# Optimization experiments

Hardware: AMD Instinct MI355X
Metric: run time of the kernel (lower is better)

## Reference

```python
import jax, jax.numpy as jnp
import numpy as np

B, S, D, H = 2, 2048, 1024, 16
HD = D // H  # 64


def setup_inputs() -> dict:
    key = jax.random.key(0)
    ks = jax.random.split(key, 10)
    sd = 1.0 / np.sqrt(D)
    return {
        "query": jax.random.normal(ks[0], (B, S, D), jnp.float32),
        "key": jax.random.normal(ks[1], (B, S, D), jnp.float32),
        "value": jax.random.normal(ks[2], (B, S, D), jnp.float32),
        "mask": jax.random.randint(ks[3], (B, S, S), 0, 2).astype(bool),
        "Wq": jax.random.normal(ks[4], (D, D), jnp.float32) * sd,
        "bq": jnp.zeros((D,), jnp.float32),
        "Wk": jax.random.normal(ks[5], (D, D), jnp.float32) * sd,
        "bk": jnp.zeros((D,), jnp.float32),
        "Wv": jax.random.normal(ks[6], (D, D), jnp.float32) * sd,
        "bv": jnp.zeros((D,), jnp.float32),
    }


def _split_heads(x, W, b):
    # nn.Linear: x @ W.T + b, then [B,S,D] -> [B*H,S,HD] (b-major, h-minor)
    h = x @ W.T + b
    h = h.reshape(B, S, H, HD).transpose(0, 2, 1, 3)  # [B,H,S,HD]
    return h.reshape(B * H, S, HD)


def reference(query, key, value, mask, Wq, bq, Wk, bk, Wv, bv):
    scale = np.sqrt(HD).astype(np.float32)
    q = _split_heads(query, Wq, bq)
    k = _split_heads(key, Wk, bk)
    v = _split_heads(value, Wv, bv)
    scores = jnp.einsum("bqd,bkd->bqk", q, k) / scale  # [B*H,S,S]
    # faithful to torch mask.repeat(H,1,1): tiles batch-major
    mask_r = jnp.tile(mask, (H, 1, 1))
    scores = jnp.where(mask_r, -jnp.inf, scores)
    attn = jax.nn.softmax(scores, axis=-1)
    ctx = jnp.einsum("bqk,bkd->bqd", attn, v)  # [B*H,S,HD]
    ctx = ctx.reshape(B, H, S, HD).transpose(0, 2, 1, 3).reshape(B, S, D)
    return ctx, attn
```

## Files before the change

### kernel.cpp

```cpp
#include <hip/hip_runtime.h>

#define B_ 2
#define S_ 2048
#define D_ 1024
#define H_ 16
#define HD_ 64
#define BH_ 32

typedef float fx4 __attribute__((ext_vector_type(4)));
typedef short s16x8 __attribute__((ext_vector_type(8)));
typedef unsigned short u16x8 __attribute__((ext_vector_type(8)));
typedef unsigned short u16x4 __attribute__((ext_vector_type(4)));

#define MFMA16(a, b, c) __builtin_amdgcn_mfma_f32_16x16x32_bf16((a), (b), (c), 0, 0, 0)

__device__ __forceinline__ unsigned short f2bf(float x) {
    unsigned u = __float_as_uint(x);
    return (unsigned short)((u + 0x7FFFu + ((u >> 16) & 1u)) >> 16);
}
__device__ __forceinline__ float bf2f(unsigned short h) {
    return __uint_as_float(((unsigned)h) << 16);
}

__global__ __launch_bounds__(256) void mask_pack(const int* __restrict__ m,
                                                 unsigned long long* __restrict__ out) {
    size_t i = (size_t)blockIdx.x * 256 + threadIdx.x;
    unsigned long long b = __ballot(m[i] != 0);
    if ((threadIdx.x & 63) == 0) out[i >> 6] = b;
}

template <int VMODE>
__global__ __launch_bounds__(256) void proj_mfma(
    const float* __restrict__ X, const float* __restrict__ W, const float* __restrict__ bias,
    unsigned short* __restrict__ o_hi, unsigned short* __restrict__ o_lo) {
    __shared__ __align__(16) unsigned short Ah[128 * 72];
    __shared__ __align__(16) unsigned short Al[128 * 72];
    __shared__ __align__(16) unsigned short Bh[64 * 72];
    __shared__ __align__(16) unsigned short Bl[64 * 72];

    const int t = threadIdx.x;
    const int n0 = blockIdx.x * 64;
    const int m0 = blockIdx.y * 128;
    const int wid = t >> 6, l = t & 63;
    const int wm = wid >> 1, wn = wid & 1;
    const int lr = l & 15, lq = l >> 4;

    fx4 acc[4][2];
#pragma unroll
    for (int i = 0; i < 4; ++i)
#pragma unroll
        for (int j = 0; j < 2; ++j) acc[i][j] = (fx4){0.f, 0.f, 0.f, 0.f};

    for (int k0 = 0; k0 < D_; k0 += 64) {
#pragma unroll
        for (int j = 0; j < 8; ++j) {
            int u = t + j * 256;
            int row = u >> 4, c4 = (u & 15) * 4;
            float4 f = *(const float4*)(X + (size_t)(m0 + row) * D_ + k0 + c4);
            unsigned short h0 = f2bf(f.x), h1 = f2bf(f.y), h2 = f2bf(f.z), h3 = f2bf(f.w);
            u16x4 hv = {h0, h1, h2, h3};
            u16x4 lv = {f2bf(f.x - bf2f(h0)), f2bf(f.y - bf2f(h1)),
                        f2bf(f.z - bf2f(h2)), f2bf(f.w - bf2f(h3))};
            *(u16x4*)(Ah + row * 72 + c4) = hv;
            *(u16x4*)(Al + row * 72 + c4) = lv;
        }
#pragma unroll
        for (int j = 0; j < 4; ++j) {
            int u = t + j * 256;
            int row = u >> 4, c4 = (u & 15) * 4;
            float4 f = *(const float4*)(W + (size_t)(n0 + row) * D_ + k0 + c4);
            unsigned short h0 = f2bf(f.x), h1 = f2bf(f.y), h2 = f2bf(f.z), h3 = f2bf(f.w);
            u16x4 hv = {h0, h1, h2, h3};
            u16x4 lv = {f2bf(f.x - bf2f(h0)), f2bf(f.y - bf2f(h1)),
                        f2bf(f.z - bf2f(h2)), f2bf(f.w - bf2f(h3))};
            *(u16x4*)(Bh + row * 72 + c4) = hv;
            *(u16x4*)(Bl + row * 72 + c4) = lv;
        }
        __syncthreads();
#pragma unroll
        for (int c = 0; c < 2; ++c) {
            s16x8 a_h[4], a_l[4];
#pragma unroll
            for (int mf = 0; mf < 4; ++mf) {
                int ro = (wm * 64 + mf * 16 + lr) * 72 + c * 32 + lq * 8;
                a_h[mf] = *(const s16x8*)(Ah + ro);
                a_l[mf] = *(const s16x8*)(Al + ro);
            }
#pragma unroll
            for (int nf = 0; nf < 2; ++nf) {
                int ro = (wn * 32 + nf * 16 + lr) * 72 + c * 32 + lq * 8;
                s16x8 b_h = *(const s16x8*)(Bh + ro);
                s16x8 b_l = *(const s16x8*)(Bl + ro);
#pragma unroll
                for (int mf = 0; mf < 4; ++mf) {
                    acc[mf][nf] = MFMA16(a_h[mf], b_h, acc[mf][nf]);
                    acc[mf][nf] = MFMA16(a_h[mf], b_l, acc[mf][nf]);
                    acc[mf][nf] = MFMA16(a_l[mf], b_h, acc[mf][nf]);
                }
            }
        }
        __syncthreads();
    }

    if (VMODE == 0) {
#pragma unroll
        for (int nf = 0; nf < 2; ++nf) {
            int n = n0 + wn * 32 + nf * 16 + lr;
            float bv = bias[n];
            int h = n >> 6, hd = n & 63;
#pragma unroll
            for (int mf = 0; mf < 4; ++mf)
#pragma unroll
                for (int r = 0; r < 4; ++r) {
                    int m = m0 + wm * 64 + mf * 16 + lq * 4 + r;
                    int b = m >> 11, s = m & 2047;
                    float v = acc[mf][nf][r] + bv;
                    size_t idx = ((size_t)((b * H_ + h) * S_ + s)) * HD_ + hd;
                    unsigned short hh = f2bf(v);
                    o_hi[idx] = hh;
                    o_lo[idx] = f2bf(v - bf2f(hh));
                }
        }
    } else {
        unsigned short* T = Ah;
#pragma unroll
        for (int nf = 0; nf < 2; ++nf) {
            int nl = wn * 32 + nf * 16 + lr;
            float bv = bias[n0 + nl];
#pragma unroll
            for (int mf = 0; mf < 4; ++mf)
#pragma unroll
                for (int r = 0; r < 4; ++r) {
                    int ml = wm * 64 + mf * 16 + lq * 4 + r;
                    T[nl * 136 + ml] = f2bf(acc[mf][nf][r] + bv);
                }
        }
        __syncthreads();
        int h = n0 >> 6, b = m0 >> 11, s0 = m0 & 2047;
        int hd = t >> 2, seg = t & 3;
        unsigned short* gp =
            o_hi + ((size_t)((b * H_ + h) * HD_ + hd)) * S_ + s0 + seg * 32;
#pragma unroll
        for (int j = 0; j < 4; ++j)
            *(u16x8*)(gp + j * 8) = *(const u16x8*)(T + hd * 136 + seg * 32 + j * 8);
    }
}

__global__ __launch_bounds__(256) void attn_mfma(
    const unsigned short* __restrict__ qh_g, const unsigned short* __restrict__ ql_g,
    const unsigned short* __restrict__ kh_g, const unsigned short* __restrict__ kl_g,
    const unsigned short* __restrict__ vt_g, const unsigned long long* __restrict__ pm,
    float* __restrict__ ctx, float* __restrict__ attn) {
    __shared__ __align__(16) unsigned short Kh[64 * 72];
    __shared__ __align__(16) unsigned short Kl[64 * 72];
    __shared__ __align__(16) unsigned short VT[64 * 72];
    __shared__ __align__(16) float E[64 * 68];

    const int t = threadIdx.x;
    const int wid = t >> 6, l = t & 63, lr = l & 15, lq = l >> 4;
    const int q0 = blockIdx.x * 64;
    const int bh = blockIdx.y;
    const size_t base = (size_t)bh * S_ * HD_;
    const size_t mrow_base = (size_t)(bh & (B_ - 1)) * S_;

    s16x8 qhi[2], qlo[2];
    {
        const unsigned short* p = qh_g + base + (size_t)(q0 + wid * 16 + lr) * HD_ + lq * 8;
        qhi[0] = *(const s16x8*)p;
        qhi[1] = *(const s16x8*)(p + 32);
        const unsigned short* p2 = ql_g + base + (size_t)(q0 + wid * 16 + lr) * HD_ + lq * 8;
        qlo[0] = *(const s16x8*)p2;
        qlo[1] = *(const s16x8*)(p2 + 32);
    }

    float rs[4] = {0.f, 0.f, 0.f, 0.f};

    for (int kt = 0; kt < S_; kt += 64) {
#pragma unroll
        for (int j = 0; j < 2; ++j) {
            int u = t + j * 256;
            int row = u >> 3, c8 = (u & 7) * 8;
            *(u16x8*)(Kh + row * 72 + c8) =
                *(const u16x8*)(kh_g + base + (size_t)(kt + row) * HD_ + c8);
        }
        __syncthreads();
        fx4 acc[4];
#pragma unroll
        for (int nt = 0; nt < 4; ++nt) acc[nt] = (fx4){0.f, 0.f, 0.f, 0.f};
#pragma unroll
        for (int c = 0; c < 2; ++c)
#pragma unroll
            for (int nt = 0; nt < 4; ++nt) {
                s16x8 kb = *(const s16x8*)(Kh + (nt * 16 + lr) * 72 + c * 32 + lq * 8);
                acc[nt] = MFMA16(qhi[c], kb, acc[nt]);
            }
        unsigned long long mw[4];
#pragma unroll
        for (int r = 0; r < 4; ++r)
            mw[r] = pm[(mrow_base + q0 + wid * 16 + lq * 4 + r) * (S_ / 64) + (kt >> 6)];
#pragma unroll
        for (int nt = 0; nt < 4; ++nt)
#pragma unroll
            for (int r = 0; r < 4; ++r) {
                float e = __expf(acc[nt][r] * 0.125f);
                e = ((mw[r] >> (nt * 16 + lr)) & 1ull) ? 0.f : e;
                rs[r] += e;
            }
        __syncthreads();
    }
#pragma unroll
    for (int off = 1; off < 16; off <<= 1)
#pragma unroll
        for (int r = 0; r < 4; ++r) rs[r] += __shfl_xor(rs[r], off, 16);
    float inv[4];
#pragma unroll
    for (int r = 0; r < 4; ++r) inv[r] = 1.f / rs[r];

    fx4 pacc[4];
#pragma unroll
    for (int dt = 0; dt < 4; ++dt) pacc[dt] = (fx4){0.f, 0.f, 0.f, 0.f};

    for (int kt = 0; kt < S_; kt += 64) {
#pragma unroll
        for (int j = 0; j < 2; ++j) {
            int u = t + j * 256;
            int row = u >> 3, c8 = (u & 7) * 8;
            *(u16x8*)(Kh + row * 72 + c8) =
                *(const u16x8*)(kh_g + base + (size_t)(kt + row) * HD_ + c8);
            *(u16x8*)(Kl + row * 72 + c8) =
                *(const u16x8*)(kl_g + base + (size_t)(kt + row) * HD_ + c8);
            *(u16x8*)(VT + row * 72 + c8) =
                *(const u16x8*)(vt_g + (size_t)(bh * HD_ + row) * S_ + kt + c8);
        }
        __syncthreads();
        fx4 acc[4];
#pragma unroll
        for (int nt = 0; nt < 4; ++nt) acc[nt] = (fx4){0.f, 0.f, 0.f, 0.f};
#pragma unroll
        for (int c = 0; c < 2; ++c)
#pragma unroll
            for (int nt = 0; nt < 4; ++nt) {
                int ro = (nt * 16 + lr) * 72 + c * 32 + lq * 8;
                s16x8 kbh = *(const s16x8*)(Kh + ro);
                s16x8 kbl = *(const s16x8*)(Kl + ro);
                acc[nt] = MFMA16(qhi[c], kbh, acc[nt]);
                acc[nt] = MFMA16(qhi[c], kbl, acc[nt]);
                acc[nt] = MFMA16(qlo[c], kbh, acc[nt]);
            }
        unsigned long long mw[4];
#pragma unroll
        for (int r = 0; r < 4; ++r)
            mw[r] = pm[(mrow_base + q0 + wid * 16 + lq * 4 + r) * (S_ / 64) + (kt >> 6)];
#pragma unroll
        for (int nt = 0; nt < 4; ++nt)
#pragma unroll
            for (int r = 0; r < 4; ++r) {
                float e = __expf(acc[nt][r] * 0.125f);
                e = ((mw[r] >> (nt * 16 + lr)) & 1ull) ? 0.f : e;
                E[(wid * 16 + lq * 4 + r) * 68 + nt * 16 + lr] = e * inv[r];
            }
        __syncthreads();
#pragma unroll
        for (int c = 0; c < 2; ++c) {
            const float* ep = E + (wid * 16 + lr) * 68 + c * 32 + lq * 8;
            fx4 p0 = *(const fx4*)ep;
            fx4 p1 = *(const fx4*)(ep + 4);
            s16x8 pa;
#pragma unroll
            for (int i = 0; i < 4; ++i) {
                pa[i] = (short)f2bf(p0[i]);
                pa[i + 4] = (short)f2bf(p1[i]);
            }
#pragma unroll
            for (int dt = 0; dt < 4; ++dt) {
                s16x8 vb = *(const s16x8*)(VT + (dt * 16 + lr) * 72 + c * 32 + lq * 8);
                pacc[dt] = MFMA16(pa, vb, pacc[dt]);
            }
        }
        {
            int rr = t >> 2, seg = t & 3;
            float* gout = attn + ((size_t)bh * S_ + q0 + rr) * S_ + kt + seg * 16;
            const float* ep2 = E + rr * 68 + seg * 16;
#pragma unroll
            for (int j = 0; j < 4; ++j) *(fx4*)(gout + j * 4) = *(const fx4*)(ep2 + j * 4);
        }
        __syncthreads();
    }

    const int b = bh >> 4, h = bh & 15;
#pragma unroll
    for (int dt = 0; dt < 4; ++dt)
#pragma unroll
        for (int r = 0; r < 4; ++r) {
            int q = q0 + wid * 16 + lq * 4 + r;
            ctx[((size_t)(b * S_ + q)) * D_ + h * HD_ + dt * 16 + lr] = pacc[dt][r];
        }
}

extern "C" void kernel_launch(void* const* d_in, const int* in_sizes, int n_in,
                              void* d_out, int out_size, void* d_ws, size_t ws_size,
                              hipStream_t stream) {
    (void)in_sizes; (void)n_in; (void)out_size; (void)ws_size;
    const float* q_in = (const float*)d_in[0];
    const float* k_in = (const float*)d_in[1];
    const float* v_in = (const float*)d_in[2];
    const int* mask = (const int*)d_in[3];
    const float* Wq = (const float*)d_in[4];
    const float* bq = (const float*)d_in[5];
    const float* Wk = (const float*)d_in[6];
    const float* bk = (const float*)d_in[7];
    const float* Wv = (const float*)d_in[8];
    const float* bv = (const float*)d_in[9];

    const size_t E_ = (size_t)BH_ * S_ * HD_;
    unsigned short* qh = (unsigned short*)d_ws;
    unsigned short* ql = qh + E_;
    unsigned short* kh = ql + E_;
    unsigned short* kl = kh + E_;
    unsigned short* vt = kl + E_;
    unsigned long long* pmask = (unsigned long long*)(vt + E_);

    float* ctx = (float*)d_out;
    float* attn = ctx + (size_t)B_ * S_ * D_;

    mask_pack<<<dim3((B_ * S_ * S_) / 256), dim3(256), 0, stream>>>(mask, pmask);

    dim3 pgrid(D_ / 64, (B_ * S_) / 128);
    proj_mfma<0><<<pgrid, dim3(256), 0, stream>>>(q_in, Wq, bq, qh, ql);
    proj_mfma<0><<<pgrid, dim3(256), 0, stream>>>(k_in, Wk, bk, kh, kl);
    proj_mfma<1><<<pgrid, dim3(256), 0, stream>>>(v_in, Wv, bv, vt, nullptr);

    dim3 agrid(S_ / 64, BH_);
    attn_mfma<<<agrid, dim3(256), 0, stream>>>(qh, ql, kh, kl, vt, pmask, ctx, attn);
}
```

Measured before the change: 1.104 ms.

## Pre-split inputs to bf16, use direct-to-LDS loads, and restructure attention tiling

Adds a conversion kernel that splits X and W into bf16 hi/lo pairs ahead of each projection. The projection GEMM then fills LDS with global_load_lds instead of converting per tile. The softmax scale times log2(e) is folded into Wq and bq so attention can call exp2 directly. V is stored in 64x64 tile-blocked layout, and attention now covers 128 queries per block (32 per wave), reading K and V straight from global memory and using only per-wave LDS for P, with wave barriers replacing block barriers. Attn values are written directly from registers. The cost is extra global traffic from the pre-converted buffers and uncoalesced per-lane attn stores.

```diff
diff --git a/kernel.cpp b/kernel.cpp
--- a/kernel.cpp
+++ b/kernel.cpp
@@ -12,7 +12,18 @@
 typedef unsigned short u16x8 __attribute__((ext_vector_type(8)));
 typedef unsigned short u16x4 __attribute__((ext_vector_type(4)));
 
+typedef __attribute__((address_space(1))) unsigned int uint_as1;
+typedef __attribute__((address_space(3))) unsigned int uint_as3;
+
 #define MFMA16(a, b, c) __builtin_amdgcn_mfma_f32_16x16x32_bf16((a), (b), (c), 0, 0, 0)
+
+#define QSCALE 0.18033688011112042f
+
+#if __has_builtin(__builtin_amdgcn_exp2f)
+#define EXP2F(x) __builtin_amdgcn_exp2f(x)
+#else
+#define EXP2F(x) exp2f(x)
+#endif
 
 __device__ __forceinline__ unsigned short f2bf(float x) {
     unsigned u = __float_as_uint(x);
@@ -20,6 +31,9 @@
 }
 __device__ __forceinline__ float bf2f(unsigned short h) {
     return __uint_as_float(((unsigned)h) << 16);
+}
+__device__ __forceinline__ void g2lds16(const unsigned short* g, unsigned short* l) {
+    __builtin_amdgcn_global_load_lds((uint_as1*)g, (uint_as3*)l, 16, 0, 0);
 }
 
 __global__ __launch_bounds__(256) void mask_pack(const int* __restrict__ m,
@@ -29,14 +43,40 @@
     if ((threadIdx.x & 63) == 0) out[i >> 6] = b;
 }
 
+__global__ __launch_bounds__(256) void cvt_pair(
+    const float* __restrict__ x, unsigned short* __restrict__ xh, unsigned short* __restrict__ xl,
+    const float* __restrict__ w, unsigned short* __restrict__ wh, unsigned short* __restrict__ wl,
+    float wscale) {
+    const int NX4 = (B_ * S_ * D_) / 4;
+    int i = blockIdx.x * 256 + threadIdx.x;
+    const float* src;
+    unsigned short* oh;
+    unsigned short* ol;
+    float sc;
+    int off;
+    if (i < NX4) { src = x; oh = xh; ol = xl; sc = 1.f; off = i; }
+    else         { src = w; oh = wh; ol = wl; sc = wscale; off = i - NX4; }
+    float4 f = ((const float4*)src)[off];
+    float a0 = f.x * sc, a1 = f.y * sc, a2 = f.z * sc, a3 = f.w * sc;
+    unsigned short h0 = f2bf(a0), h1 = f2bf(a1), h2 = f2bf(a2), h3 = f2bf(a3);
+    u16x4 hv = {h0, h1, h2, h3};
+    u16x4 lv = {f2bf(a0 - bf2f(h0)), f2bf(a1 - bf2f(h1)), f2bf(a2 - bf2f(h2)),
+                f2bf(a3 - bf2f(h3))};
+    *(u16x4*)(oh + (size_t)off * 4) = hv;
+    *(u16x4*)(ol + (size_t)off * 4) = lv;
+}
+
 template <int VMODE>
 __global__ __launch_bounds__(256) void proj_mfma(
-    const float* __restrict__ X, const float* __restrict__ W, const float* __restrict__ bias,
+    const unsigned short* __restrict__ Xh, const unsigned short* __restrict__ Xl,
+    const unsigned short* __restrict__ Wh, const unsigned short* __restrict__ Wl,
+    const float* __restrict__ bias, float bscale,
     unsigned short* __restrict__ o_hi, unsigned short* __restrict__ o_lo) {
-    __shared__ __align__(16) unsigned short Ah[128 * 72];
-    __shared__ __align__(16) unsigned short Al[128 * 72];
-    __shared__ __align__(16) unsigned short Bh[64 * 72];
-    __shared__ __align__(16) unsigned short Bl[64 * 72];
+    __shared__ __align__(16) unsigned short smem[24576];
+    unsigned short* Ah = smem;
+    unsigned short* Al = smem + 8192;
+    unsigned short* Bh = smem + 16384;
+    unsigned short* Bl = smem + 20480;
 
     const int t = threadIdx.x;
     const int n0 = blockIdx.x * 64;
@@ -53,28 +93,20 @@
 
     for (int k0 = 0; k0 < D_; k0 += 64) {
 #pragma unroll
-        for (int j = 0; j < 8; ++j) {
-            int u = t + j * 256;
-            int row = u >> 4, c4 = (u & 15) * 4;
-            float4 f = *(const float4*)(X + (size_t)(m0 + row) * D_ + k0 + c4);
-            unsigned short h0 = f2bf(f.x), h1 = f2bf(f.y), h2 = f2bf(f.z), h3 = f2bf(f.w);
-            u16x4 hv = {h0, h1, h2, h3};
-            u16x4 lv = {f2bf(f.x - bf2f(h0)), f2bf(f.y - bf2f(h1)),
-                        f2bf(f.z - bf2f(h2)), f2bf(f.w - bf2f(h3))};
-            *(u16x4*)(Ah + row * 72 + c4) = hv;
-            *(u16x4*)(Al + row * 72 + c4) = lv;
-        }
-#pragma unroll
         for (int j = 0; j < 4; ++j) {
             int u = t + j * 256;
-            int row = u >> 4, c4 = (u & 15) * 4;
-            float4 f = *(const float4*)(W + (size_t)(n0 + row) * D_ + k0 + c4);
-            unsigned short h0 = f2bf(f.x), h1 = f2bf(f.y), h2 = f2bf(f.z), h3 = f2bf(f.w);
-            u16x4 hv = {h0, h1, h2, h3};
-            u16x4 lv = {f2bf(f.x - bf2f(h0)), f2bf(f.y - bf2f(h1)),
-                        f2bf(f.z - bf2f(h2)), f2bf(f.w - bf2f(h3))};
-            *(u16x4*)(Bh + row * 72 + c4) = hv;
-            *(u16x4*)(Bl + row * 72 + c4) = lv;
+            int row = u >> 3, cu = u & 7;
+            size_t go = (size_t)(m0 + row) * D_ + k0 + cu * 8;
+            g2lds16(Xh + go, Ah + u * 8);
+            g2lds16(Xl + go, Al + u * 8);
+        }
+#pragma unroll
+        for (int j = 0; j < 2; ++j) {
+            int u = t + j * 256;
+            int row = u >> 3, cu = u & 7;
+            size_t go = (size_t)(n0 + row) * D_ + k0 + cu * 8;
+            g2lds16(Wh + go, Bh + u * 8);
+            g2lds16(Wl + go, Bl + u * 8);
         }
         __syncthreads();
 #pragma unroll
@@ -82,13 +114,13 @@
             s16x8 a_h[4], a_l[4];
 #pragma unroll
             for (int mf = 0; mf < 4; ++mf) {
-                int ro = (wm * 64 + mf * 16 + lr) * 72 + c * 32 + lq * 8;
+                int ro = (wm * 64 + mf * 16 + lr) * 64 + c * 32 + lq * 8;
                 a_h[mf] = *(const s16x8*)(Ah + ro);
                 a_l[mf] = *(const s16x8*)(Al + ro);
             }
 #pragma unroll
             for (int nf = 0; nf < 2; ++nf) {
-                int ro = (wn * 32 + nf * 16 + lr) * 72 + c * 32 + lq * 8;
+                int ro = (wn * 32 + nf * 16 + lr) * 64 + c * 32 + lq * 8;
                 s16x8 b_h = *(const s16x8*)(Bh + ro);
                 s16x8 b_l = *(const s16x8*)(Bl + ro);
 #pragma unroll
@@ -106,7 +138,7 @@
 #pragma unroll
         for (int nf = 0; nf < 2; ++nf) {
             int n = n0 + wn * 32 + nf * 16 + lr;
-            float bv = bias[n];
+            float bv = bias[n] * bscale;
             int h = n >> 6, hd = n & 63;
 #pragma unroll
             for (int mf = 0; mf < 4; ++mf)
@@ -122,11 +154,11 @@
                 }
         }
     } else {
-        unsigned short* T = Ah;
+        unsigned short* T = smem;
 #pragma unroll
         for (int nf = 0; nf < 2; ++nf) {
             int nl = wn * 32 + nf * 16 + lr;
-            float bv = bias[n0 + nl];
+            float bv = bias[n0 + nl] * bscale;
 #pragma unroll
             for (int mf = 0; mf < 4; ++mf)
 #pragma unroll
@@ -137,12 +169,13 @@
         }
         __syncthreads();
         int h = n0 >> 6, b = m0 >> 11, s0 = m0 & 2047;
+        int bhv = b * H_ + h;
         int hd = t >> 2, seg = t & 3;
-        unsigned short* gp =
-            o_hi + ((size_t)((b * H_ + h) * HD_ + hd)) * S_ + s0 + seg * 32;
+        size_t vb0 = ((size_t)(bhv * 32 + (s0 >> 6) + (seg >> 1))) * 4096 +
+                     (size_t)hd * 64 + (seg & 1) * 32;
 #pragma unroll
         for (int j = 0; j < 4; ++j)
-            *(u16x8*)(gp + j * 8) = *(const u16x8*)(T + hd * 136 + seg * 32 + j * 8);
+            *(u16x8*)(o_hi + vb0 + j * 8) = *(const u16x8*)(T + hd * 136 + seg * 32 + j * 8);
     }
 }
 
@@ -150,151 +183,145 @@
     const unsigned short* __restrict__ qh_g, const unsigned short* __restrict__ ql_g,
     const unsigned short* __restrict__ kh_g, const unsigned short* __restrict__ kl_g,
     const unsigned short* __restrict__ vt_g, const unsigned long long* __restrict__ pm,
-    float* __restrict__ ctx, float* __restrict__ attn) {
-    __shared__ __align__(16) unsigned short Kh[64 * 72];
-    __shared__ __align__(16) unsigned short Kl[64 * 72];
-    __shared__ __align__(16) unsigned short VT[64 * 72];
-    __shared__ __align__(16) float E[64 * 68];
+    float* __restrict__ out_ctx, float* __restrict__ out_attn) {
+    __shared__ __align__(16) unsigned short Ew[4 * 32 * 72];
 
     const int t = threadIdx.x;
     const int wid = t >> 6, l = t & 63, lr = l & 15, lq = l >> 4;
-    const int q0 = blockIdx.x * 64;
+    const int q0 = blockIdx.x * 128;
     const int bh = blockIdx.y;
     const size_t base = (size_t)bh * S_ * HD_;
-    const size_t mrow_base = (size_t)(bh & (B_ - 1)) * S_;
-
-    s16x8 qhi[2], qlo[2];
-    {
-        const unsigned short* p = qh_g + base + (size_t)(q0 + wid * 16 + lr) * HD_ + lq * 8;
-        qhi[0] = *(const s16x8*)p;
-        qhi[1] = *(const s16x8*)(p + 32);
-        const unsigned short* p2 = ql_g + base + (size_t)(q0 + wid * 16 + lr) * HD_ + lq * 8;
-        qlo[0] = *(const s16x8*)p2;
-        qlo[1] = *(const s16x8*)(p2 + 32);
-    }
-
-    float rs[4] = {0.f, 0.f, 0.f, 0.f};
+    const int qr = q0 + wid * 32;
+    const size_t mrow0 = (size_t)(bh & (B_ - 1)) * S_ + qr;
+    unsigned short* ew = Ew + wid * 32 * 72;
+
+    s16x8 qhi[2][2], qlo[2][2];
+#pragma unroll
+    for (int mt = 0; mt < 2; ++mt) {
+        const unsigned short* qp = qh_g + base + (size_t)(qr + mt * 16 + lr) * HD_ + lq * 8;
+        qhi[mt][0] = *(const s16x8*)qp;
+        qhi[mt][1] = *(const s16x8*)(qp + 32);
+        const unsigned short* qp2 = ql_g + base + (size_t)(qr + mt * 16 + lr) * HD_ + lq * 8;
+        qlo[mt][0] = *(const s16x8*)qp2;
+        qlo[mt][1] = *(const s16x8*)(qp2 + 32);
+    }
+
+    float rs[2][4] = {};
 
     for (int kt = 0; kt < S_; kt += 64) {
-#pragma unroll
-        for (int j = 0; j < 2; ++j) {
-            int u = t + j * 256;
-            int row = u >> 3, c8 = (u & 7) * 8;
-            *(u16x8*)(Kh + row * 72 + c8) =
-                *(const u16x8*)(kh_g + base + (size_t)(kt + row) * HD_ + c8);
-        }
-        __syncthreads();
-        fx4 acc[4];
-#pragma unroll
-        for (int nt = 0; nt < 4; ++nt) acc[nt] = (fx4){0.f, 0.f, 0.f, 0.f};
+        const unsigned short* kp = kh_g + base + (size_t)(kt + lr) * HD_ + lq * 8;
+        fx4 acc[2][4];
+#pragma unroll
+        for (int mt = 0; mt < 2; ++mt)
+#pragma unroll
+            for (int nt = 0; nt < 4; ++nt) acc[mt][nt] = (fx4){0.f, 0.f, 0.f, 0.f};
 #pragma unroll
         for (int c = 0; c < 2; ++c)
 #pragma unroll
             for (int nt = 0; nt < 4; ++nt) {
-                s16x8 kb = *(const s16x8*)(Kh + (nt * 16 + lr) * 72 + c * 32 + lq * 8);
-                acc[nt] = MFMA16(qhi[c], kb, acc[nt]);
-            }
-        unsigned long long mw[4];
-#pragma unroll
-        for (int r = 0; r < 4; ++r)
-            mw[r] = pm[(mrow_base + q0 + wid * 16 + lq * 4 + r) * (S_ / 64) + (kt >> 6)];
-#pragma unroll
-        for (int nt = 0; nt < 4; ++nt)
+                s16x8 kb = *(const s16x8*)(kp + nt * 16 * HD_ + c * 32);
+                acc[0][nt] = MFMA16(qhi[0][c], kb, acc[0][nt]);
+                acc[1][nt] = MFMA16(qhi[1][c], kb, acc[1][nt]);
+            }
+#pragma unroll
+        for (int mt = 0; mt < 2; ++mt) {
+            unsigned long long mw[4];
+#pragma unroll
+            for (int r = 0; r < 4; ++r)
+                mw[r] = pm[(mrow0 + mt * 16 + lq * 4 + r) * (S_ / 64) + (kt >> 6)];
+#pragma unroll
+            for (int nt = 0; nt < 4; ++nt)
+#pragma unroll
+                for (int r = 0; r < 4; ++r) {
+                    float e = EXP2F(acc[mt][nt][r]);
+                    e = ((mw[r] >> (nt * 16 + lr)) & 1ull) ? 0.f : e;
+                    rs[mt][r] += e;
+                }
+        }
+    }
+#pragma unroll
+    for (int off = 1; off < 16; off <<= 1)
+#pragma unroll
+        for (int mt = 0; mt < 2; ++mt)
+#pragma unroll
+            for (int r = 0; r < 4; ++r) rs[mt][r] += __shfl_xor(rs[mt][r], off, 16);
+    float inv[2][4];
+#pragma unroll
+    for (int mt = 0; mt < 2; ++mt)
+#pragma unroll
+        for (int r = 0; r < 4; ++r) inv[mt][r] = 1.f / rs[mt][r];
+
+    fx4 pacc[2][4];
+#pragma unroll
+    for (int mt = 0; mt < 2; ++mt)
+#pragma unroll
+        for (int dt = 0; dt < 4; ++dt) pacc[mt][dt] = (fx4){0.f, 0.f, 0.f, 0.f};
+
+    for (int kt = 0; kt < S_; kt += 64) {
+        const unsigned short* kph = kh_g + base + (size_t)(kt + lr) * HD_ + lq * 8;
+        const unsigned short* kpl = kl_g + base + (size_t)(kt + lr) * HD_ + lq * 8;
+        fx4 acc[2][4];
+#pragma unroll
+        for (int mt = 0; mt < 2; ++mt)
+#pragma unroll
+            for (int nt = 0; nt < 4; ++nt) acc[mt][nt] = (fx4){0.f, 0.f, 0.f, 0.f};
+#pragma unroll
+        for (int c = 0; c < 2; ++c)
+#pragma unroll
+            for (int nt = 0; nt < 4; ++nt) {
+                s16x8 kbh = *(const s16x8*)(kph + nt * 16 * HD_ + c * 32);
+                s16x8 kbl = *(const s16x8*)(kpl + nt * 16 * HD_ + c * 32);
+#pragma unroll
+                for (int mt = 0; mt < 2; ++mt) {
+                    acc[mt][nt] = MFMA16(qhi[mt][c], kbh, acc[mt][nt]);
+                    acc[mt][nt] = MFMA16(qhi[mt][c], kbl, acc[mt][nt]);
+                    acc[mt][nt] = MFMA16(qlo[mt][c], kbh, acc[mt][nt]);
+                }
+            }
+#pragma unroll
+        for (int mt = 0; mt < 2; ++mt) {
+            unsigned long long mw[4];
+#pragma unroll
+            for (int r = 0; r < 4; ++r)
+                mw[r] = pm[(mrow0 + mt * 16 + lq * 4 + r) * (S_ / 64) + (kt >> 6)];
+            float* ap = out_attn + ((size_t)bh * S_ + qr + mt * 16 + lq * 4) * S_ + kt + lr;
+#pragma unroll
+            for (int nt = 0; nt < 4; ++nt)
+#pragma unroll
+                for (int r = 0; r < 4; ++r) {
+                    float e = EXP2F(acc[mt][nt][r]);
+                    e = ((mw[r] >> (nt * 16 + lr)) & 1ull) ? 0.f : e * inv[mt][r];
+                    ap[(size_t)r * S_ + nt * 16] = e;
+                    ew[(mt * 16 + lq * 4 + r) * 72 + nt * 16 + lr] = f2bf(e);
+                }
+        }
+        __builtin_amdgcn_wave_barrier();
+        const unsigned short* vp = vt_g + ((size_t)(bh * 32 + (kt >> 6))) * 4096;
+#pragma unroll
+        for (int c = 0; c < 2; ++c) {
+            s16x8 pa0 = *(const s16x8*)(ew + lr * 72 + c * 32 + lq * 8);
+            s16x8 pa1 = *(const s16x8*)(ew + (16 + lr) * 72 + c * 32 + lq * 8);
+#pragma unroll
+            for (int dt = 0; dt < 4; ++dt) {
+                s16x8 vb = *(const s16x8*)(vp + (dt * 16 + lr) * 64 + c * 32 + lq * 8);
+                pacc[0][dt] = MFMA16(pa0, vb, pacc[0][dt]);
+                pacc[1][dt] = MFMA16(pa1, vb, pacc[1][dt]);
+            }
+        }
+        __builtin_amdgcn_wave_barrier();
+    }
+
+    const int b = bh >> 4, h = bh & 15;
+#pragma unroll
+    for (int mt = 0; mt < 2; ++mt)
+#pragma unroll
+        for (int dt = 0; dt < 4; ++dt)
 #pragma unroll
             for (int r = 0; r < 4; ++r) {
-                float e = __expf(acc[nt][r] * 0.125f);
-                e = ((mw[r] >> (nt * 16 + lr)) & 1ull) ? 0.f : e;
-                rs[r] += e;
-            }
-        __syncthreads();
-    }
-#pragma unroll
-    for (int off = 1; off < 16; off <<= 1)
-#pragma unroll
-        for (int r = 0; r < 4; ++r) rs[r] += __shfl_xor(rs[r], off, 16);
-    float inv[4];
-#pragma unroll
-    for (int r = 0; r < 4; ++r) inv[r] = 1.f / rs[r];
-
-    fx4 pacc[4];
-#pragma unroll
-    for (int dt = 0; dt < 4; ++dt) pacc[dt] = (fx4){0.f, 0.f, 0.f, 0.f};
-
-    for (int kt = 0; kt < S_; kt += 64) {
-#pragma unroll
-        for (int j = 0; j < 2; ++j) {
-            int u = t + j * 256;
-            int row = u >> 3, c8 = (u & 7) * 8;
-            *(u16x8*)(Kh + row * 72 + c8) =
-                *(const u16x8*)(kh_g + base + (size_t)(kt + row) * HD_ + c8);
-            *(u16x8*)(Kl + row * 72 + c8) =
-                *(const u16x8*)(kl_g + base + (size_t)(kt + row) * HD_ + c8);
-            *(u16x8*)(VT + row * 72 + c8) =
-                *(const u16x8*)(vt_g + (size_t)(bh * HD_ + row) * S_ + kt + c8);
-        }
-        __syncthreads();
-        fx4 acc[4];
-#pragma unroll
-        for (int nt = 0; nt < 4; ++nt) acc[nt] = (fx4){0.f, 0.f, 0.f, 0.f};
-#pragma unroll
-        for (int c = 0; c < 2; ++c)
-#pragma unroll
-            for (int nt = 0; nt < 4; ++nt) {
-                int ro = (nt * 16 + lr) * 72 + c * 32 + lq * 8;
-                s16x8 kbh = *(const s16x8*)(Kh + ro);
-                s16x8 kbl = *(const s16x8*)(Kl + ro);
-                acc[nt] = MFMA16(qhi[c], kbh, acc[nt]);
-                acc[nt] = MFMA16(qhi[c], kbl, acc[nt]);
-                acc[nt] = MFMA16(qlo[c], kbh, acc[nt]);
-            }
-        unsigned long long mw[4];
-#pragma unroll
-        for (int r = 0; r < 4; ++r)
-            mw[r] = pm[(mrow_base + q0 + wid * 16 + lq * 4 + r) * (S_ / 64) + (kt >> 6)];
-#pragma unroll
-        for (int nt = 0; nt < 4; ++nt)
-#pragma unroll
-            for (int r = 0; r < 4; ++r) {
-                float e = __expf(acc[nt][r] * 0.125f);
-                e = ((mw[r] >> (nt * 16 + lr)) & 1ull) ? 0.f : e;
-                E[(wid * 16 + lq * 4 + r) * 68 + nt * 16 + lr] = e * inv[r];
-            }
-        __syncthreads();
-#pragma unroll
-        for (int c = 0; c < 2; ++c) {
-            const float* ep = E + (wid * 16 + lr) * 68 + c * 32 + lq * 8;
-            fx4 p0 = *(const fx4*)ep;
-            fx4 p1 = *(const fx4*)(ep + 4);
-            s16x8 pa;
-#pragma unroll
-            for (int i = 0; i < 4; ++i) {
-                pa[i] = (short)f2bf(p0[i]);
-                pa[i + 4] = (short)f2bf(p1[i]);
-            }
-#pragma unroll
-            for (int dt = 0; dt < 4; ++dt) {
-                s16x8 vb = *(const s16x8*)(VT + (dt * 16 + lr) * 72 + c * 32 + lq * 8);
-                pacc[dt] = MFMA16(pa, vb, pacc[dt]);
-            }
-        }
-        {
-            int rr = t >> 2, seg = t & 3;
-            float* gout = attn + ((size_t)bh * S_ + q0 + rr) * S_ + kt + seg * 16;
-            const float* ep2 = E + rr * 68 + seg * 16;
-#pragma unroll
-            for (int j = 0; j < 4; ++j) *(fx4*)(gout + j * 4) = *(const fx4*)(ep2 + j * 4);
-        }
-        __syncthreads();
-    }
-
-    const int b = bh >> 4, h = bh & 15;
-#pragma unroll
-    for (int dt = 0; dt < 4; ++dt)
-#pragma unroll
-        for (int r = 0; r < 4; ++r) {
-            int q = q0 + wid * 16 + lq * 4 + r;
-            ctx[((size_t)(b * S_ + q)) * D_ + h * HD_ + dt * 16 + lr] = pacc[dt][r];
-        }
+                int q = qr + mt * 16 + lq * 4 + r;
+                out_ctx[((size_t)(b * S_ + q)) * D_ + h * HD_ + dt * 16 + lr] =
+                    pacc[mt][dt][r];
+            }
 }
 
 extern "C" void kernel_launch(void* const* d_in, const int* in_sizes, int n_in,
@@ -313,23 +340,35 @@
     const float* bv = (const float*)d_in[9];
 
     const size_t E_ = (size_t)BH_ * S_ * HD_;
+    const size_t WE_ = (size_t)D_ * D_;
     unsigned short* qh = (unsigned short*)d_ws;
     unsigned short* ql = qh + E_;
     unsigned short* kh = ql + E_;
     unsigned short* kl = kh + E_;
     unsigned short* vt = kl + E_;
-    unsigned long long* pmask = (unsigned long long*)(vt + E_);
+    unsigned short* Xh = vt + E_;
+    unsigned short* Xl = Xh + E_;
+    unsigned short* Wh = Xl + E_;
+    unsigned short* Wl = Wh + WE_;
+    unsigned long long* pmask = (unsigned long long*)(Wl + WE_);
 
     float* ctx = (float*)d_out;
     float* attn = ctx + (size_t)B_ * S_ * D_;
 
     mask_pack<<<dim3((B_ * S_ * S_) / 256), dim3(256), 0, stream>>>(mask, pmask);
 
+    const int CG = ((B_ * S_ * D_) / 4 + (D_ * D_) / 4) / 256;
     dim3 pgrid(D_ / 64, (B_ * S_) / 128);
-    proj_mfma<0><<<pgrid, dim3(256), 0, stream>>>(q_in, Wq, bq, qh, ql);
-    proj_mfma<0><<<pgrid, dim3(256), 0, stream>>>(k_in, Wk, bk, kh, kl);
-    proj_mfma<1><<<pgrid, dim3(256), 0, stream>>>(v_in, Wv, bv, vt, nullptr);
-
-    dim3 agrid(S_ / 64, BH_);
+
+    cvt_pair<<<dim3(CG), dim3(256), 0, stream>>>(q_in, Xh, Xl, Wq, Wh, Wl, QSCALE);
+    proj_mfma<0><<<pgrid, dim3(256), 0, stream>>>(Xh, Xl, Wh, Wl, bq, QSCALE, qh, ql);
+
+    cvt_pair<<<dim3(CG), dim3(256), 0, stream>>>(k_in, Xh, Xl, Wk, Wh, Wl, 1.0f);
+    proj_mfma<0><<<pgrid, dim3(256), 0, stream>>>(Xh, Xl, Wh, Wl, bk, 1.0f, kh, kl);
+
+    cvt_pair<<<dim3(CG), dim3(256), 0, stream>>>(v_in, Xh, Xl, Wv, Wh, Wl, 1.0f);
+    proj_mfma<1><<<pgrid, dim3(256), 0, stream>>>(Xh, Xl, Wh, Wl, bv, 1.0f, vt, nullptr);
+
+    dim3 agrid(S_ / 128, BH_);
     attn_mfma<<<agrid, dim3(256), 0, stream>>>(qh, ql, kh, kl, vt, pmask, ctx, attn);
 }
```

Measured after the change: 1.004 ms. 9.0% less time.
